# Performance work log

Measured on AMD Instinct MI355X. Metric: run time of the kernel, lower is better.

The kernel has to match this reference:

```python
import math
import jax
import jax.numpy as jnp
import numpy as np

DECAY_RATE = 0.99
LOG_CLAMP_MIN = -10.0


def setup_inputs() -> dict:
    key = jax.random.key(0)
    k0, k1, k2, k3, k4, k5 = jax.random.split(key, 6)
    B, S, D, N = 32, 4096, 256, 64
    return {
        "query": jax.random.normal(k0, (B, S, D), dtype=jnp.float32),
        "memory": jax.random.normal(k1, (1, N, D), dtype=jnp.float32),
        "importance": jax.random.uniform(k2, (1, N), dtype=jnp.float32),
        "age": jax.random.uniform(k3, (1, N), dtype=jnp.float32) * 10.0,
        # torch.nn.Linear weights are [out_features, in_features]; applied as x @ W.T
        "W_q": jax.random.normal(k4, (D, D), dtype=jnp.float32) / jnp.sqrt(D).astype(jnp.float32),
        "W_k": jax.random.normal(k5, (D, D), dtype=jnp.float32) / jnp.sqrt(D).astype(jnp.float32),
        "top_k": 8,
    }


def reference(query, memory, importance, age, W_q, W_k, top_k):
    # MemoryBank.read(): top-k masked attention over a small memory bank
    # query: [B, S, D]; memory: [1, N, D]; importance/age: [1, N]
    D = query.shape[-1]
    N = memory.shape[1]
    mem = memory[0]          # [N, D] (buffer is batch-broadcast in torch via expand)

    q = query @ W_q.T                      # [B, S, D]
    k = mem @ W_k.T                        # [N, D]
    scores = jnp.einsum("bsd,nd->bsn", q, k) / jnp.sqrt(jnp.asarray(D, query.dtype))

    # importance-decay bias, log-clamped at -10
    eff_imp = importance[0] * (DECAY_RATE ** age[0])           # [N]
    scores = scores + jnp.maximum(jnp.log(eff_imp), LOG_CLAMP_MIN)[None, None, :]

    if top_k < N:
        _, topk_idx = jax.lax.top_k(scores, top_k)             # [B, S, k]
        # scatter 1.0 at top-k indices (N is small, one-hot sum is cheap)
        mask = jax.nn.one_hot(topk_idx, N, dtype=scores.dtype).sum(axis=-2)  # [B, S, N]
        scores = jnp.where(mask > 0, scores, -jnp.inf)

    attn_weights = jax.nn.softmax(scores, axis=-1)             # [B, S, N]
    retrieved = jnp.einsum("bsn,nd->bsd", attn_weights, mem)   # [B, S, D]
    return retrieved, attn_weights
```

## Files before the change

kernel.cpp:

```cpp
#include <hip/hip_runtime.h>
#include <hip/hip_bf16.h>

#define DD 256
#define NM 64

typedef unsigned long long u64;
typedef float v2f __attribute__((ext_vector_type(2)));

struct v2x2 { v2f lo, hi; };
static __device__ __forceinline__ v2x2 splitf4(float4 f) {
    union { float4 a; v2x2 b; } u; u.a = f; return u.b;
}

#define PK_FMA_SPLATLO(acc, q2, c2) \
    asm("v_pk_fma_f32 %0, %1, %2, %0 op_sel:[0,0,0] op_sel_hi:[0,1,1]" \
        : "+v"(acc) : "v"(q2), "v"(c2))
#define PK_FMA_SPLATHI(acc, q2, c2) \
    asm("v_pk_fma_f32 %0, %1, %2, %0 op_sel:[1,0,0] op_sel_hi:[1,1,1]" \
        : "+v"(acc) : "v"(q2), "v"(c2))
#define PK_FMA_SPLATLO_S(acc, q2, c2) \
    asm("v_pk_fma_f32 %0, %1, %2, %0 op_sel:[0,0,0] op_sel_hi:[0,1,1]" \
        : "+v"(acc) : "v"(q2), "s"(c2))
#define PK_FMA_SPLATHI_S(acc, q2, c2) \
    asm("v_pk_fma_f32 %0, %1, %2, %0 op_sel:[1,0,0] op_sel_hi:[1,1,1]" \
        : "+v"(acc) : "v"(q2), "s"(c2))

__global__ __launch_bounds__(256) void prep_tr(
    const float* __restrict__ Wq, const float* __restrict__ Wk,
    float* __restrict__ wqt, float* __restrict__ wkt)
{
    const int o = blockIdx.x;
    const int d = threadIdx.x;
    if (blockIdx.y == 0) wqt[d * DD + o] = Wq[o * DD + d];
    else                 wkt[d * DD + o] = Wk[o * DD + d];
}

__global__ __launch_bounds__(256) void prep_kT(
    const float* __restrict__ mem, const float* __restrict__ wkt,
    const float* __restrict__ imp, const float* __restrict__ age,
    float* __restrict__ kT8, float* __restrict__ bias)
{
    const int n = blockIdx.x;
    const int o = threadIdx.x;
    const float* mrow = mem + n * DD;
    float acc = 0.f;
    for (int d = 0; d < DD; ++d)
        acc = fmaf(mrow[d], wkt[d * DD + o], acc);
    kT8[(o >> 2) * 256 + (n >> 1) * 8 + (o & 3) * 2 + (n & 1)] = acc;

    if (o == 0) {
        double eff = (double)imp[n] * pow(0.99, (double)age[n]);
        float b = (float)log(eff);
        if (!(b >= -10.0f)) b = -10.0f;
        bias[n] = b;
    }
}

__global__ __launch_bounds__(256, 2) void qgemm(
    const float* __restrict__ query,
    const float4* __restrict__ wqt4,
    float* __restrict__ qout,
    int M)
{
    __shared__ float lds[32 * DD];
    const int t = threadIdx.x;
    const int l = t & 63;
    const int w = __builtin_amdgcn_readfirstlane((int)(t >> 6));
    const int row0 = blockIdx.x * 32;

    {
        const float4* q4g = reinterpret_cast<const float4*>(query);
#pragma unroll
        for (int i = 0; i < 8; ++i) {
            const int idx = i * 256 + t;
            const int r = idx >> 6, c4 = idx & 63;
            int gr = row0 + r; if (gr > M - 1) gr = M - 1;
            *reinterpret_cast<float4*>(&lds[r * DD + c4 * 4]) =
                q4g[(size_t)gr * 64 + c4];
        }
    }
    __syncthreads();

    v2f a01[8], a23[8];
#pragma unroll
    for (int rr = 0; rr < 8; ++rr) { a01[rr] = (v2f)(0.f); a23[rr] = (v2f)(0.f); }

    {
        float4 cw0 = wqt4[0 * NM + l];
        float4 cw1 = wqt4[1 * NM + l];
        float4 cw2 = wqt4[2 * NM + l];
        float4 cw3 = wqt4[3 * NM + l];

        const float* qbase = &lds[(w * 8) * DD];

        for (int d0 = 0; d0 < DD; d0 += 4) {
            const int dn = (d0 + 4) & (DD - 1);
            const float4 nw0 = wqt4[(dn + 0) * NM + l];
            const float4 nw1 = wqt4[(dn + 1) * NM + l];
            const float4 nw2 = wqt4[(dn + 2) * NM + l];
            const float4 nw3 = wqt4[(dn + 3) * NM + l];
            const v2x2 c0 = splitf4(cw0), c1 = splitf4(cw1);
            const v2x2 c2 = splitf4(cw2), c3 = splitf4(cw3);
#pragma unroll
            for (int rr = 0; rr < 8; ++rr) {
                const float4 qq = *reinterpret_cast<const float4*>(
                    qbase + rr * DD + d0);
                const v2x2 qh = splitf4(qq);
                PK_FMA_SPLATLO(a01[rr], qh.lo, c0.lo);
                PK_FMA_SPLATLO(a23[rr], qh.lo, c0.hi);
                PK_FMA_SPLATHI(a01[rr], qh.lo, c1.lo);
                PK_FMA_SPLATHI(a23[rr], qh.lo, c1.hi);
                PK_FMA_SPLATLO(a01[rr], qh.hi, c2.lo);
                PK_FMA_SPLATLO(a23[rr], qh.hi, c2.hi);
                PK_FMA_SPLATHI(a01[rr], qh.hi, c3.lo);
                PK_FMA_SPLATHI(a23[rr], qh.hi, c3.hi);
            }
            cw0 = nw0; cw1 = nw1; cw2 = nw2; cw3 = nw3;
        }
    }

#pragma unroll
    for (int rr = 0; rr < 8; ++rr) {
        const int grow = row0 + w * 8 + rr;
        if (grow < M) {
            float4 v; v.x = a01[rr].x; v.y = a01[rr].y; v.z = a23[rr].x; v.w = a23[rr].y;
            *reinterpret_cast<float4*>(&qout[(size_t)grow * DD + 4 * l]) = v;
        }
    }
}

__global__ __launch_bounds__(256, 2) void mb_fin(
    const float* __restrict__ qin,
    const float* __restrict__ mem,
    const float* __restrict__ kT8,
    const float* __restrict__ bias,
    const int* __restrict__ topk_p,
    float* __restrict__ out_ret,
    float* __restrict__ out_attn,
    int M)
{
    __shared__ float lds[64 * DD];
    float* s_f   = lds;
    int*   sel_i = (int*)(lds + 64 * NM);
    float* sel_w = lds + 64 * NM + 64 * 16;

    const int t = threadIdx.x;
    const int l = t & 63;
    const int w = __builtin_amdgcn_readfirstlane((int)(t >> 6));
    const int row0 = blockIdx.x * 64;
    const int k = *topk_p;

    {
        const float4* q4g = reinterpret_cast<const float4*>(qin);
#pragma unroll
        for (int i = 0; i < 16; ++i) {
            const int idx = i * 256 + t;
            const int r = idx >> 6, c4 = idx & 63;
            int gr = row0 + r; if (gr > M - 1) gr = M - 1;
            *reinterpret_cast<float4*>(&lds[r * DD + ((c4 ^ r) & 63) * 4]) =
                q4g[(size_t)gr * 64 + c4];
        }
    }
    __syncthreads();

    const int nb = w * 16;
    v2f p[8];
    {
#pragma unroll
        for (int j2 = 0; j2 < 8; ++j2) p[j2] = (v2f)(0.f);

        const v2f* kt2base = reinterpret_cast<const v2f*>(kT8) + w * 32;

        for (int og = 0; og < DD / 4; ++og) {
            const float4 q4 = *reinterpret_cast<const float4*>(
                &lds[l * DD + (((og ^ l) & 63) << 2)]);
            const v2x2 qh = splitf4(q4);
            const v2f* kt2 = kt2base + og * 128;
#pragma unroll
            for (int j2 = 0; j2 < 8; ++j2) {
                const v2f k0 = kt2[j2 * 4 + 0];
                const v2f k1 = kt2[j2 * 4 + 1];
                const v2f k2 = kt2[j2 * 4 + 2];
                const v2f k3 = kt2[j2 * 4 + 3];
                PK_FMA_SPLATLO_S(p[j2], qh.lo, k0);
                PK_FMA_SPLATHI_S(p[j2], qh.lo, k1);
                PK_FMA_SPLATLO_S(p[j2], qh.hi, k2);
                PK_FMA_SPLATHI_S(p[j2], qh.hi, k3);
            }
        }
    }
    __syncthreads();

#pragma unroll
    for (int j2 = 0; j2 < 8; ++j2) {
        const int n0 = nb + 2 * j2;
        s_f[l * NM + ((n0     + l) & 63)] = p[j2].x * 0.0625f + bias[n0];
        s_f[l * NM + ((n0 + 1 + l) & 63)] = p[j2].y * 0.0625f + bias[n0 + 1];
    }
    __syncthreads();

    if (w == 0) {
        const int r = l;
        float sv[NM];
#pragma unroll
        for (int n = 0; n < NM; ++n) sv[n] = s_f[r * NM + ((n + r) & 63)];

        if (k < NM) {
            const int kk = k < 16 ? k : 16;
            u64 taken = 0ull;
            float mmax = 0.f, Z = 0.f;
            for (int i = 0; i < kk; ++i) {
                float m = -1.0e30f;
                int idx = 0;
#pragma unroll
                for (int n = 0; n < NM; ++n) {
                    const bool avail  = ((taken >> n) & 1ull) == 0ull;
                    const bool better = avail && (sv[n] > m);
                    m   = better ? sv[n] : m;
                    idx = better ? n : idx;
                }
                taken |= (1ull << idx);
                if (i == 0) mmax = m;
                const float wv = expf(m - mmax);
                Z += wv;
                sel_i[r * 16 + i] = idx;
                sel_w[r * 16 + i] = wv;
            }
#pragma unroll
            for (int n = 0; n < NM; ++n) s_f[r * NM + ((n + r) & 63)] = 0.f;
            for (int i = 0; i < kk; ++i) {
                const float wz = sel_w[r * 16 + i] / Z;
                sel_w[r * 16 + i] = wz;
                s_f[r * NM + ((sel_i[r * 16 + i] + r) & 63)] = wz;
            }
        } else {
            float m = -1.0e30f;
#pragma unroll
            for (int n = 0; n < NM; ++n) m = sv[n] > m ? sv[n] : m;
            float Z = 0.f;
#pragma unroll
            for (int n = 0; n < NM; ++n) Z += expf(sv[n] - m);
#pragma unroll
            for (int n = 0; n < NM; ++n) s_f[r * NM + ((n + r) & 63)] = expf(sv[n] - m) / Z;
        }
    }
    __syncthreads();

#pragma unroll
    for (int it = 0; it < 16; ++it) {
        const int idx  = it * 256 + t;
        const int r    = idx >> 6, n = idx & 63;
        const int grow = row0 + r;
        if (grow < M) out_attn[(size_t)grow * NM + n] = s_f[r * NM + ((n + r) & 63)];
    }

    {
        const float4* mem4 = reinterpret_cast<const float4*>(mem);
        const int kk = k < 16 ? k : 16;
#pragma unroll 1
        for (int rr = 0; rr < 16; ++rr) {
            const int r    = w * 16 + rr;
            const int grow = row0 + r;
            if (grow >= M) continue;
            float4 acc; acc.x = 0.f; acc.y = 0.f; acc.z = 0.f; acc.w = 0.f;
            if (k < NM) {
                for (int i = 0; i < kk; ++i) {
                    const int   mi = sel_i[r * 16 + i];
                    const float wz = sel_w[r * 16 + i];
                    const float4 mv = mem4[mi * 64 + l];
                    acc.x = fmaf(wz, mv.x, acc.x);
                    acc.y = fmaf(wz, mv.y, acc.y);
                    acc.z = fmaf(wz, mv.z, acc.z);
                    acc.w = fmaf(wz, mv.w, acc.w);
                }
            } else {
                for (int n = 0; n < NM; ++n) {
                    const float wz = s_f[r * NM + ((n + r) & 63)];
                    const float4 mv = mem4[n * 64 + l];
                    acc.x = fmaf(wz, mv.x, acc.x);
                    acc.y = fmaf(wz, mv.y, acc.y);
                    acc.z = fmaf(wz, mv.z, acc.z);
                    acc.w = fmaf(wz, mv.w, acc.w);
                }
            }
            *reinterpret_cast<float4*>(&out_ret[(size_t)grow * DD + 4 * l]) = acc;
        }
    }
}

extern "C" void kernel_launch(void* const* d_in, const int* in_sizes, int n_in,
                              void* d_out, int out_size, void* d_ws, size_t ws_size,
                              hipStream_t stream) {
    const float* query      = (const float*)d_in[0];
    const float* memory     = (const float*)d_in[1];
    const float* importance = (const float*)d_in[2];
    const float* age        = (const float*)d_in[3];
    const float* Wq         = (const float*)d_in[4];
    const float* Wk         = (const float*)d_in[5];
    const int*   topk       = (const int*)d_in[6];

    const int M = in_sizes[0] / DD;

    float* kT8  = (float*)d_ws;
    float* bias = kT8 + (size_t)DD * NM;
    float* wqt  = bias + 64;
    float* wkt  = wqt + (size_t)DD * DD;

    hipLaunchKernelGGL(prep_tr, dim3(DD, 2), dim3(DD), 0, stream,
                       Wq, Wk, wqt, wkt);
    hipLaunchKernelGGL(prep_kT, dim3(NM), dim3(DD), 0, stream,
                       memory, wkt, importance, age, kT8, bias);

    float* out_ret  = (float*)d_out;
    float* out_attn = out_ret + (size_t)M * DD;

    hipLaunchKernelGGL(qgemm, dim3((M + 31) / 32), dim3(256), 0, stream,
                       query, (const float4*)wqt, out_ret, M);
    hipLaunchKernelGGL(mb_fin, dim3((M + 63) / 64), dim3(256), 0, stream,
                       out_ret, memory, kT8, bias, topk, out_ret, out_attn, M);
}
```

Measured before the change: 415.3 us.

## Switch both main kernels to single-wave 8-row blocks with lane-per-memory-slot scores

Both the query projection and the finalisation kernel now run one 64-lane wave per block, handling 8 rows instead of 32 or 64. In the finalisation kernel each lane computes the score for one memory slot across the 8 rows, using a new float4 key layout, instead of the packed FMAs on scalar-broadcast keys. The intent is to shrink LDS use and cut block-wide barriers so more waves fit per CU. The cost is more blocks with less work each, the top-k step now runs on only 8 of 64 lanes, and the Wq and key weights are re-fetched per 8 rows, raising cache traffic.

```diff
diff --git a/kernel.cpp b/kernel.cpp
--- a/kernel.cpp
+++ b/kernel.cpp
@@ -18,12 +18,6 @@
 #define PK_FMA_SPLATHI(acc, q2, c2) \
     asm("v_pk_fma_f32 %0, %1, %2, %0 op_sel:[1,0,0] op_sel_hi:[1,1,1]" \
         : "+v"(acc) : "v"(q2), "v"(c2))
-#define PK_FMA_SPLATLO_S(acc, q2, c2) \
-    asm("v_pk_fma_f32 %0, %1, %2, %0 op_sel:[0,0,0] op_sel_hi:[0,1,1]" \
-        : "+v"(acc) : "v"(q2), "s"(c2))
-#define PK_FMA_SPLATHI_S(acc, q2, c2) \
-    asm("v_pk_fma_f32 %0, %1, %2, %0 op_sel:[1,0,0] op_sel_hi:[1,1,1]" \
-        : "+v"(acc) : "v"(q2), "s"(c2))
 
 __global__ __launch_bounds__(256) void prep_tr(
     const float* __restrict__ Wq, const float* __restrict__ Wk,
@@ -38,7 +32,7 @@
 __global__ __launch_bounds__(256) void prep_kT(
     const float* __restrict__ mem, const float* __restrict__ wkt,
     const float* __restrict__ imp, const float* __restrict__ age,
-    float* __restrict__ kT8, float* __restrict__ bias)
+    float* __restrict__ kT4, float* __restrict__ bias)
 {
     const int n = blockIdx.x;
     const int o = threadIdx.x;
@@ -46,7 +40,7 @@
     float acc = 0.f;
     for (int d = 0; d < DD; ++d)
         acc = fmaf(mrow[d], wkt[d * DD + o], acc);
-    kT8[(o >> 2) * 256 + (n >> 1) * 8 + (o & 3) * 2 + (n & 1)] = acc;
+    kT4[(o >> 2) * (NM * 4) + n * 4 + (o & 3)] = acc;
 
     if (o == 0) {
         double eff = (double)imp[n] * pow(0.99, (double)age[n]);
@@ -56,27 +50,23 @@
     }
 }
 
-__global__ __launch_bounds__(256, 2) void qgemm(
+__global__ __launch_bounds__(64, 2) void qgemm_w(
     const float* __restrict__ query,
     const float4* __restrict__ wqt4,
     float* __restrict__ qout,
     int M)
 {
-    __shared__ float lds[32 * DD];
-    const int t = threadIdx.x;
-    const int l = t & 63;
-    const int w = __builtin_amdgcn_readfirstlane((int)(t >> 6));
-    const int row0 = blockIdx.x * 32;
+    __shared__ float lds[8 * DD];
+    const int l = threadIdx.x;
+    const int row0 = blockIdx.x * 8;
 
     {
         const float4* q4g = reinterpret_cast<const float4*>(query);
 #pragma unroll
-        for (int i = 0; i < 8; ++i) {
-            const int idx = i * 256 + t;
-            const int r = idx >> 6, c4 = idx & 63;
-            int gr = row0 + r; if (gr > M - 1) gr = M - 1;
-            *reinterpret_cast<float4*>(&lds[r * DD + c4 * 4]) =
-                q4g[(size_t)gr * 64 + c4];
+        for (int rr = 0; rr < 8; ++rr) {
+            int gr = row0 + rr; if (gr > M - 1) gr = M - 1;
+            *reinterpret_cast<float4*>(&lds[rr * DD + l * 4]) =
+                q4g[(size_t)gr * 64 + l];
         }
     }
     __syncthreads();
@@ -90,8 +80,6 @@
         float4 cw1 = wqt4[1 * NM + l];
         float4 cw2 = wqt4[2 * NM + l];
         float4 cw3 = wqt4[3 * NM + l];
-
-        const float* qbase = &lds[(w * 8) * DD];
 
         for (int d0 = 0; d0 < DD; d0 += 4) {
             const int dn = (d0 + 4) & (DD - 1);
@@ -104,7 +92,7 @@
 #pragma unroll
             for (int rr = 0; rr < 8; ++rr) {
                 const float4 qq = *reinterpret_cast<const float4*>(
-                    qbase + rr * DD + d0);
+                    &lds[rr * DD + d0]);
                 const v2x2 qh = splitf4(qq);
                 PK_FMA_SPLATLO(a01[rr], qh.lo, c0.lo);
                 PK_FMA_SPLATLO(a23[rr], qh.lo, c0.hi);
@@ -121,7 +109,7 @@
 
 #pragma unroll
     for (int rr = 0; rr < 8; ++rr) {
-        const int grow = row0 + w * 8 + rr;
+        const int grow = row0 + rr;
         if (grow < M) {
             float4 v; v.x = a01[rr].x; v.y = a01[rr].y; v.z = a23[rr].x; v.w = a23[rr].y;
             *reinterpret_cast<float4*>(&qout[(size_t)grow * DD + 4 * l]) = v;
@@ -129,81 +117,68 @@
     }
 }
 
-__global__ __launch_bounds__(256, 2) void mb_fin(
+__global__ __launch_bounds__(64, 2) void fin_w(
     const float* __restrict__ qin,
     const float* __restrict__ mem,
-    const float* __restrict__ kT8,
+    const float4* __restrict__ kT44,
     const float* __restrict__ bias,
     const int* __restrict__ topk_p,
     float* __restrict__ out_ret,
     float* __restrict__ out_attn,
     int M)
 {
-    __shared__ float lds[64 * DD];
-    float* s_f   = lds;
-    int*   sel_i = (int*)(lds + 64 * NM);
-    float* sel_w = lds + 64 * NM + 64 * 16;
-
-    const int t = threadIdx.x;
-    const int l = t & 63;
-    const int w = __builtin_amdgcn_readfirstlane((int)(t >> 6));
-    const int row0 = blockIdx.x * 64;
+    __shared__ float lds_q[8 * DD];
+    __shared__ float lds_s[8 * NM];
+    int*   sel_i = (int*)lds_q;
+    float* sel_w = lds_q + 8 * 16;
+
+    const int l = threadIdx.x;
+    const int row0 = blockIdx.x * 8;
     const int k = *topk_p;
 
     {
         const float4* q4g = reinterpret_cast<const float4*>(qin);
 #pragma unroll
-        for (int i = 0; i < 16; ++i) {
-            const int idx = i * 256 + t;
-            const int r = idx >> 6, c4 = idx & 63;
-            int gr = row0 + r; if (gr > M - 1) gr = M - 1;
-            *reinterpret_cast<float4*>(&lds[r * DD + ((c4 ^ r) & 63) * 4]) =
-                q4g[(size_t)gr * 64 + c4];
-        }
-    }
-    __syncthreads();
-
-    const int nb = w * 16;
-    v2f p[8];
-    {
-#pragma unroll
-        for (int j2 = 0; j2 < 8; ++j2) p[j2] = (v2f)(0.f);
-
-        const v2f* kt2base = reinterpret_cast<const v2f*>(kT8) + w * 32;
+        for (int rr = 0; rr < 8; ++rr) {
+            int gr = row0 + rr; if (gr > M - 1) gr = M - 1;
+            *reinterpret_cast<float4*>(&lds_q[rr * DD + l * 4]) =
+                q4g[(size_t)gr * 64 + l];
+        }
+    }
+    __syncthreads();
+
+    {
+        const int n = l;
+        const float bn = bias[n];
+        float sc[8];
+#pragma unroll
+        for (int r = 0; r < 8; ++r) sc[r] = 0.f;
 
         for (int og = 0; og < DD / 4; ++og) {
-            const float4 q4 = *reinterpret_cast<const float4*>(
-                &lds[l * DD + (((og ^ l) & 63) << 2)]);
-            const v2x2 qh = splitf4(q4);
-            const v2f* kt2 = kt2base + og * 128;
-#pragma unroll
-            for (int j2 = 0; j2 < 8; ++j2) {
-                const v2f k0 = kt2[j2 * 4 + 0];
-                const v2f k1 = kt2[j2 * 4 + 1];
-                const v2f k2 = kt2[j2 * 4 + 2];
-                const v2f k3 = kt2[j2 * 4 + 3];
-                PK_FMA_SPLATLO_S(p[j2], qh.lo, k0);
-                PK_FMA_SPLATHI_S(p[j2], qh.lo, k1);
-                PK_FMA_SPLATLO_S(p[j2], qh.hi, k2);
-                PK_FMA_SPLATHI_S(p[j2], qh.hi, k3);
-            }
-        }
-    }
-    __syncthreads();
-
-#pragma unroll
-    for (int j2 = 0; j2 < 8; ++j2) {
-        const int n0 = nb + 2 * j2;
-        s_f[l * NM + ((n0     + l) & 63)] = p[j2].x * 0.0625f + bias[n0];
-        s_f[l * NM + ((n0 + 1 + l) & 63)] = p[j2].y * 0.0625f + bias[n0 + 1];
-    }
-    __syncthreads();
-
-    if (w == 0) {
+            const float4 kt = kT44[og * NM + n];
+#pragma unroll
+            for (int r = 0; r < 8; ++r) {
+                const float4 q4 = *reinterpret_cast<const float4*>(
+                    &lds_q[r * DD + og * 4]);
+                float v = sc[r];
+                v = fmaf(q4.x, kt.x, v);
+                v = fmaf(q4.y, kt.y, v);
+                v = fmaf(q4.z, kt.z, v);
+                v = fmaf(q4.w, kt.w, v);
+                sc[r] = v;
+            }
+        }
+#pragma unroll
+        for (int r = 0; r < 8; ++r)
+            lds_s[r * NM + ((n + r) & 63)] = sc[r] * 0.0625f + bn;
+    }
+    __syncthreads();
+
+    if (l < 8) {
         const int r = l;
         float sv[NM];
 #pragma unroll
-        for (int n = 0; n < NM; ++n) sv[n] = s_f[r * NM + ((n + r) & 63)];
+        for (int n = 0; n < NM; ++n) sv[n] = lds_s[r * NM + ((n + r) & 63)];
 
         if (k < NM) {
             const int kk = k < 16 ? k : 16;
@@ -227,11 +202,11 @@
                 sel_w[r * 16 + i] = wv;
             }
 #pragma unroll
-            for (int n = 0; n < NM; ++n) s_f[r * NM + ((n + r) & 63)] = 0.f;
+            for (int n = 0; n < NM; ++n) lds_s[r * NM + ((n + r) & 63)] = 0.f;
             for (int i = 0; i < kk; ++i) {
                 const float wz = sel_w[r * 16 + i] / Z;
                 sel_w[r * 16 + i] = wz;
-                s_f[r * NM + ((sel_i[r * 16 + i] + r) & 63)] = wz;
+                lds_s[r * NM + ((sel_i[r * 16 + i] + r) & 63)] = wz;
             }
         } else {
             float m = -1.0e30f;
@@ -241,25 +216,22 @@
 #pragma unroll
             for (int n = 0; n < NM; ++n) Z += expf(sv[n] - m);
 #pragma unroll
-            for (int n = 0; n < NM; ++n) s_f[r * NM + ((n + r) & 63)] = expf(sv[n] - m) / Z;
-        }
-    }
-    __syncthreads();
-
-#pragma unroll
-    for (int it = 0; it < 16; ++it) {
-        const int idx  = it * 256 + t;
-        const int r    = idx >> 6, n = idx & 63;
+            for (int n = 0; n < NM; ++n) lds_s[r * NM + ((n + r) & 63)] = expf(sv[n] - m) / Z;
+        }
+    }
+    __syncthreads();
+
+#pragma unroll
+    for (int r = 0; r < 8; ++r) {
         const int grow = row0 + r;
-        if (grow < M) out_attn[(size_t)grow * NM + n] = s_f[r * NM + ((n + r) & 63)];
+        if (grow < M) out_attn[(size_t)grow * NM + l] = lds_s[r * NM + ((l + r) & 63)];
     }
 
     {
         const float4* mem4 = reinterpret_cast<const float4*>(mem);
         const int kk = k < 16 ? k : 16;
 #pragma unroll 1
-        for (int rr = 0; rr < 16; ++rr) {
-            const int r    = w * 16 + rr;
+        for (int r = 0; r < 8; ++r) {
             const int grow = row0 + r;
             if (grow >= M) continue;
             float4 acc; acc.x = 0.f; acc.y = 0.f; acc.z = 0.f; acc.w = 0.f;
@@ -275,7 +247,7 @@
                 }
             } else {
                 for (int n = 0; n < NM; ++n) {
-                    const float wz = s_f[r * NM + ((n + r) & 63)];
+                    const float wz = lds_s[r * NM + ((n + r) & 63)];
                     const float4 mv = mem4[n * 64 + l];
                     acc.x = fmaf(wz, mv.x, acc.x);
                     acc.y = fmaf(wz, mv.y, acc.y);
@@ -301,21 +273,23 @@
 
     const int M = in_sizes[0] / DD;
 
-    float* kT8  = (float*)d_ws;
-    float* bias = kT8 + (size_t)DD * NM;
+    float* kT4  = (float*)d_ws;
+    float* bias = kT4 + (size_t)DD * NM;
     float* wqt  = bias + 64;
     float* wkt  = wqt + (size_t)DD * DD;
 
     hipLaunchKernelGGL(prep_tr, dim3(DD, 2), dim3(DD), 0, stream,
                        Wq, Wk, wqt, wkt);
     hipLaunchKernelGGL(prep_kT, dim3(NM), dim3(DD), 0, stream,
-                       memory, wkt, importance, age, kT8, bias);
+                       memory, wkt, importance, age, kT4, bias);
 
     float* out_ret  = (float*)d_out;
     float* out_attn = out_ret + (size_t)M * DD;
 
-    hipLaunchKernelGGL(qgemm, dim3((M + 31) / 32), dim3(256), 0, stream,
+    const int nblk = (M + 7) / 8;
+    hipLaunchKernelGGL(qgemm_w, dim3(nblk), dim3(64), 0, stream,
                        query, (const float4*)wqt, out_ret, M);
-    hipLaunchKernelGGL(mb_fin, dim3((M + 63) / 64), dim3(256), 0, stream,
-                       out_ret, memory, kT8, bias, topk, out_ret, out_attn, M);
-}
+    hipLaunchKernelGGL(fin_w, dim3(nblk), dim3(64), 0, stream,
+                       out_ret, memory, (const float4*)kT4, bias, topk,
+                       out_ret, out_attn, M);
+}
```

Result: slower. 440.2 us (+6.0%).
